# Optimization experiments

Measured on AMD Instinct MI355X. Metric: run time of the kernel, lower is better.

Reference implementation:

```python
import jax, jax.numpy as jnp
import numpy as np

B, F, T, K = 32, 256, 2048, 1024


def setup_inputs() -> dict:
    key = jax.random.key(0)
    k1, k2 = jax.random.split(key)
    x = jax.random.normal(k1, (B, F, T), dtype=jnp.float32)
    emb_weight = jax.random.normal(k2, (K, F), dtype=jnp.float32)
    return {"x": x, "emb_weight": emb_weight}


def reference(x, emb_weight):
    # x: [B, F, T] -> [B, T, F]
    xt = jnp.swapaxes(x, -1, -2)
    nf = xt.shape[-1]

    def sq_dist(a, c):
        # mean over feature dim of (a - c)^2, expanded to avoid a [B,T,K,F]
        # broadcast tensor: (|a|^2 - 2 a.c + |c|^2) / F -> [B, T, K]
        a2 = jnp.sum(a * a, axis=-1, keepdims=True)          # [B,T,1]
        c2 = jnp.sum(c * c, axis=-1)                          # [K]
        ac = jnp.einsum('btf,kf->btk', a, c)                  # [B,T,K]
        return (a2 - 2.0 * ac + c2) / nf

    w_sg = jax.lax.stop_gradient(emb_weight)
    x_sg = jax.lax.stop_gradient(xt)

    dist = sq_dist(xt, w_sg)                                  # [B,T,K]
    min_dist = jnp.min(dist, axis=-1)                         # [B,T]
    idxs = jnpp_argmin(dist) if False else jnp.argmin(dist, axis=-1)  # [B,T]

    loss_commit = min_dist.mean()                              # grads -> x only
    loss_codebook = jnp.min(sq_dist(x_sg, emb_weight), axis=-1).mean()  # grads -> codebook only

    out = w_sg[idxs]                                           # [B,T,F] gather (detached)
    out = jnp.swapaxes(out, -1, -2)                            # [B,F,T]
    return out, loss_commit, loss_codebook
```

## Files before the change

kernel.cpp:

```cpp
#include <hip/hip_runtime.h>

#define B_ 32
#define F_ 256
#define T_ 2048
#define K_ 1024
#define M_ (B_*T_)

#define MARGIN 0.45f
#define CAP 512

typedef _Float16 f16x8 __attribute__((ext_vector_type(8)));
typedef float f32x4 __attribute__((ext_vector_type(4)));

__global__ void k_prep(const float* __restrict__ emb, unsigned short* __restrict__ cprep,
                       double* __restrict__ c2d, float* __restrict__ c2f) {
    int k = blockIdx.x;
    int l = threadIdx.x;
    float4 v = *reinterpret_cast<const float4*>(emb + k * F_ + l * 4);
    union { _Float16 h[4]; unsigned long long ll; } cv;
    cv.h[0] = (_Float16)v.x; cv.h[1] = (_Float16)v.y;
    cv.h[2] = (_Float16)v.z; cv.h[3] = (_Float16)v.w;
    *reinterpret_cast<unsigned long long*>(cprep + k * F_ + l * 4) = cv.ll;
    double s = (double)v.x * v.x + (double)v.y * v.y
             + (double)v.z * v.z + (double)v.w * v.w;
    #pragma unroll
    for (int d = 1; d < 64; d <<= 1) s += __shfl_xor(s, d);
    if (l == 0) { c2d[k] = s; c2f[k] = (float)s; }
}

__global__ __launch_bounds__(256, 2) void k_argmin(
    const float* __restrict__ x, const float* __restrict__ emb,
    const unsigned short* __restrict__ cprep,
    const double* __restrict__ c2d, const float* __restrict__ c2f,
    int* __restrict__ idx_out, double* __restrict__ partials)
{
    __shared__ __align__(16) unsigned char bbuf[2][8192];
    __shared__ int cand_cnt;
    __shared__ int cand_pk[CAP];
    __shared__ double cand_q[CAP];
    __shared__ int res_k[128];
    __shared__ double redbuf[256];

    const int tid = threadIdx.x;
    const int bid = blockIdx.x;
    const int b = bid >> 4;
    const int t_base = (bid & 15) * 128;
    const int w = tid >> 6;
    const int l = tid & 63;
    const int row = l & 15;
    const int qd = l >> 4;
    const int rsw = (row & 7) << 4;
    const int row512 = row * 512;

    if (tid == 0) cand_cnt = 0;

    const float* xb = x + (size_t)b * (F_ * T_) + t_base + w * 32 + row
                    + (size_t)qd * 8 * T_;
    float xsql = 0.f, xsqh = 0.f;
    f16x8 ah0[8], ah1[8];
    #pragma unroll
    for (int s = 0; s < 8; ++s) {
        #pragma unroll
        for (int j = 0; j < 8; ++j) {
            size_t fo = (size_t)(s * 32 + j) * T_;
            float v0 = xb[fo];
            float v1 = xb[fo + 16];
            ah0[s][j] = (_Float16)v0;
            ah1[s][j] = (_Float16)v1;
            xsql = fmaf(v0, v0, xsql);
            xsqh = fmaf(v1, v1, xsqh);
        }
    }
    float xl = xsql, xh = xsqh;
    xl += __shfl_xor(xl, 16); xl += __shfl_xor(xl, 32);
    xh += __shfl_xor(xh, 16); xh += __shfl_xor(xh, 32);
    float a2s[8];
    #pragma unroll
    for (int r = 0; r < 4; ++r) {
        a2s[r]     = __shfl(xl, qd * 4 + r);
        a2s[4 + r] = __shfl(xh, qd * 4 + r);
    }

    const int srow = tid >> 5;
    const int sfc = tid & 31;
    const int sdst = srow * 512 + ((sfc * 16) ^ ((srow & 7) << 4));

    {
        const unsigned short* p0 = cprep + srow * F_ + sfc * 8;
        uint4 a = *reinterpret_cast<const uint4*>(p0);
        uint4 c = *reinterpret_cast<const uint4*>(p0 + 8 * F_);
        *reinterpret_cast<uint4*>(&bbuf[0][sdst]) = a;
        *reinterpret_cast<uint4*>(&bbuf[0][sdst + 4096]) = c;
    }
    __syncthreads();

    int m1i[8], m2i[8], m3i[8];
    #pragma unroll
    for (int i = 0; i < 8; ++i) { m1i[i] = 0x7FFFFFFF; m2i[i] = 0x7FFFFFFF; m3i[i] = 0x7FFFFFFF; }

    for (int tile = 0; tile < 64; ++tile) {
        const int cur = tile & 1, nxt = cur ^ 1;
        uint4 st0, st1;
        if (tile < 63) {
            const unsigned short* p0 = cprep + ((tile + 1) * 16 + srow) * F_ + sfc * 8;
            st0 = *reinterpret_cast<const uint4*>(p0);
            st1 = *reinterpret_cast<const uint4*>(p0 + 8 * F_);
        }
        const int kk = tile * 16 + row;
        float c2v = c2f[kk];

        f32x4 acc0 = {0.f, 0.f, 0.f, 0.f};
        f32x4 acc1 = {0.f, 0.f, 0.f, 0.f};
        #pragma unroll
        for (int s = 0; s < 8; ++s) {
            int off = row512 + (((s * 64) + qd * 16) ^ rsw);
            f16x8 bh = *reinterpret_cast<const f16x8*>(&bbuf[cur][off]);
            acc0 = __builtin_amdgcn_mfma_f32_16x16x32_f16(ah0[s], bh, acc0, 0, 0, 0);
            acc1 = __builtin_amdgcn_mfma_f32_16x16x32_f16(ah1[s], bh, acc1, 0, 0, 0);
        }

        #pragma unroll
        for (int r = 0; r < 4; ++r) {
            {
                float q = fmaf(acc0[r], -2.0f, c2v + a2s[r]);
                int vi = (__float_as_int(q) & 0xFFFFFC00) | kk;
                int t1 = max(m1i[r], vi); m1i[r] = min(m1i[r], vi);
                int t2 = max(m2i[r], t1); m2i[r] = min(m2i[r], t1);
                m3i[r] = min(m3i[r], t2);
            }
            {
                float q = fmaf(acc1[r], -2.0f, c2v + a2s[4 + r]);
                int vi = (__float_as_int(q) & 0xFFFFFC00) | kk;
                int t1 = max(m1i[4 + r], vi); m1i[4 + r] = min(m1i[4 + r], vi);
                int t2 = max(m2i[4 + r], t1); m2i[4 + r] = min(m2i[4 + r], t1);
                m3i[4 + r] = min(m3i[4 + r], t2);
            }
        }

        if (tile < 63) {
            *reinterpret_cast<uint4*>(&bbuf[nxt][sdst]) = st0;
            *reinterpret_cast<uint4*>(&bbuf[nxt][sdst + 4096]) = st1;
        }
        __syncthreads();
    }

    double loss_acc = 0.0;
    #pragma unroll
    for (int i = 0; i < 8; ++i) {
        int gm = m1i[i];
        #pragma unroll
        for (int d = 1; d < 16; d <<= 1) { int o = __shfl_xor(gm, d); gm = min(gm, o); }
        float thr = __int_as_float(gm & 0xFFFFFC00) + MARGIN;
        bool in1 = __int_as_float(m1i[i] & 0xFFFFFC00) <= thr;
        bool in2 = __int_as_float(m2i[i] & 0xFFFFFC00) <= thr;
        bool in3 = __int_as_float(m3i[i] & 0xFFFFFC00) <= thr;
        unsigned long long b1 = __ballot(in1), b2 = __ballot(in2), b3 = __ballot(in3);
        int sh = l & 48;
        int cnt = __popcll((b1 >> sh) & 0xFFFFull) + __popcll((b2 >> sh) & 0xFFFFull)
                + __popcll((b3 >> sh) & 0xFFFFull);
        int p = w * 32 + (i >> 2) * 16 + qd * 4 + (i & 3);
        if ((l & 15) == 0) {
            res_k[p] = gm & 1023;
            loss_acc += (double)__int_as_float((gm & 0xFFFFFC00) | 512);
        }
        if (cnt >= 2) {
            if (in1) { int s_ = atomicAdd(&cand_cnt, 1); if (s_ < CAP) cand_pk[s_] = (p << 10) | (m1i[i] & 1023); }
            if (in2) { int s_ = atomicAdd(&cand_cnt, 1); if (s_ < CAP) cand_pk[s_] = (p << 10) | (m2i[i] & 1023); }
            if (in3) { int s_ = atomicAdd(&cand_cnt, 1); if (s_ < CAP) cand_pk[s_] = (p << 10) | (m3i[i] & 1023); }
        }
    }
    __syncthreads();

    int total = cand_cnt; if (total > CAP) total = CAP;
    for (int ci = w; ci < total; ci += 4) {
        int pk = cand_pk[ci];
        int p = pk >> 10, k = pk & 1023;
        const float* xp = x + (size_t)b * (F_ * T_) + t_base + p;
        const float4 ev = *reinterpret_cast<const float4*>(emb + k * F_ + l * 4);
        double s = 0.0;
        s += (double)xp[(size_t)(l * 4 + 0) * T_] * (double)ev.x;
        s += (double)xp[(size_t)(l * 4 + 1) * T_] * (double)ev.y;
        s += (double)xp[(size_t)(l * 4 + 2) * T_] * (double)ev.z;
        s += (double)xp[(size_t)(l * 4 + 3) * T_] * (double)ev.w;
        #pragma unroll
        for (int d = 1; d < 64; d <<= 1) s += __shfl_xor(s, d);
        if (l == 0) cand_q[ci] = c2d[k] - 2.0 * s;
    }
    __syncthreads();

    if (tid < 128) {
        double bq = 1e300; int bk = -1; bool any = false;
        for (int ci = 0; ci < total; ++ci) {
            int pk = cand_pk[ci];
            if ((pk >> 10) == tid) {
                double q = cand_q[ci]; int k = pk & 1023;
                if (q < bq || (q == bq && k < bk)) { bq = q; bk = k; }
                any = true;
            }
        }
        idx_out[b * T_ + t_base + tid] = any ? bk : res_k[tid];
    }

    redbuf[tid] = loss_acc;
    __syncthreads();
    for (int s = 128; s > 0; s >>= 1) {
        if (tid < s) redbuf[tid] += redbuf[tid + s];
        __syncthreads();
    }
    if (tid == 0) partials[bid] = redbuf[0];
}

__global__ void k_loss(const double* __restrict__ partials, float* __restrict__ out_losses) {
    __shared__ double redd[256];
    int tid = threadIdx.x;
    redd[tid] = partials[tid] + partials[tid + 256];
    __syncthreads();
    for (int s = 128; s > 0; s >>= 1) {
        if (tid < s) redd[tid] += redd[tid + s];
        __syncthreads();
    }
    if (tid == 0) {
        float loss = (float)(redd[0] / ((double)F_ * (double)M_));
        out_losses[0] = loss;
        out_losses[1] = loss;
    }
}

__global__ void k_gather(const float* __restrict__ emb, const int* __restrict__ idx,
                         float* __restrict__ out) {
    int gid = blockIdx.x * 256 + threadIdx.x;
    int t4 = gid & 511;
    int f = (gid >> 9) & 255;
    int b = gid >> 17;
    const int4 ip = *reinterpret_cast<const int4*>(idx + b * T_ + t4 * 4);
    float4 v;
    v.x = emb[ip.x * F_ + f];
    v.y = emb[ip.y * F_ + f];
    v.z = emb[ip.z * F_ + f];
    v.w = emb[ip.w * F_ + f];
    *reinterpret_cast<float4*>(out + (b * F_ + f) * T_ + t4 * 4) = v;
}

extern "C" void kernel_launch(void* const* d_in, const int* in_sizes, int n_in,
                              void* d_out, int out_size, void* d_ws, size_t ws_size,
                              hipStream_t stream) {
    const float* x   = (const float*)d_in[0];
    const float* emb = (const float*)d_in[1];
    float* out = (float*)d_out;

    double* c2d = (double*)d_ws;
    double* partials = c2d + K_;
    unsigned short* cprep = (unsigned short*)(partials + 512);
    float* c2f = (float*)(cprep + K_ * F_);
    int* idx = (int*)(c2f + K_);

    k_prep<<<K_, 64, 0, stream>>>(emb, cprep, c2d, c2f);
    k_argmin<<<M_ / 128, 256, 0, stream>>>(x, emb, cprep, c2d, c2f, idx, partials);
    k_loss<<<1, 256, 0, stream>>>(partials, out + (size_t)M_ * F_);
    k_gather<<<(M_ * (F_ / 4)) / 256, 256, 0, stream>>>(emb, idx, out);
}
```

Measured before the change: 203.3 us.

## Use single-wave argmin blocks with register-prefetched codebook and LDS-transposed gather

Argmin blocks shrink from four waves to one, each handling 32 positions. The codebook tiles now go straight from global memory into registers with a two-tile software prefetch, so the LDS double buffer and per-tile block barriers are gone. The gather kernel now reads whole contiguous codebook rows into an LDS tile and writes transposed coalesced output, replacing scattered per-element reads. The trade-offs are more codebook traffic through L2, since each wave loads every tile itself, a smaller candidate cap, and more partials to reduce in the loss kernel.

Result: slower. 244.9 us (+20.5%).

```diff
diff --git a/kernel.cpp b/kernel.cpp
--- a/kernel.cpp
+++ b/kernel.cpp
@@ -7,7 +7,7 @@
 #define M_ (B_*T_)
 
 #define MARGIN 0.45f
-#define CAP 512
+#define CAP 128
 
 typedef _Float16 f16x8 __attribute__((ext_vector_type(8)));
 typedef float f32x4 __attribute__((ext_vector_type(4)));
@@ -28,34 +28,63 @@
     if (l == 0) { c2d[k] = s; c2f[k] = (float)s; }
 }
 
-__global__ __launch_bounds__(256, 2) void k_argmin(
+#define LOADB(dst, c2n, tt) {                                                    \
+    const unsigned short* bp = cprep + ((tt) * 16 + row) * F_ + qd * 8;          \
+    _Pragma("unroll")                                                            \
+    for (int s_ = 0; s_ < 8; ++s_)                                               \
+        dst[s_] = *reinterpret_cast<const f16x8*>(bp + s_ * 32);                 \
+    c2n = c2f[(tt) * 16 + row];                                                  \
+}
+
+#define COMPUTE(bf, c2v, tt) {                                                   \
+    const int kk = (tt) * 16 + row;                                              \
+    f32x4 acc0 = {0.f, 0.f, 0.f, 0.f};                                           \
+    f32x4 acc1 = {0.f, 0.f, 0.f, 0.f};                                           \
+    _Pragma("unroll")                                                            \
+    for (int s_ = 0; s_ < 8; ++s_) {                                             \
+        acc0 = __builtin_amdgcn_mfma_f32_16x16x32_f16(ah0[s_], bf[s_], acc0, 0, 0, 0); \
+        acc1 = __builtin_amdgcn_mfma_f32_16x16x32_f16(ah1[s_], bf[s_], acc1, 0, 0, 0); \
+    }                                                                            \
+    _Pragma("unroll")                                                            \
+    for (int r_ = 0; r_ < 4; ++r_) {                                             \
+        {                                                                        \
+            float q = fmaf(acc0[r_], -2.0f, c2v + a2s[r_]);                      \
+            int vi = (__float_as_int(q) & 0xFFFFFC00) | kk;                      \
+            int t1 = max(m1i[r_], vi); m1i[r_] = min(m1i[r_], vi);               \
+            int t2 = max(m2i[r_], t1); m2i[r_] = min(m2i[r_], t1);               \
+            m3i[r_] = min(m3i[r_], t2);                                          \
+        }                                                                        \
+        {                                                                        \
+            float q = fmaf(acc1[r_], -2.0f, c2v + a2s[4 + r_]);                  \
+            int vi = (__float_as_int(q) & 0xFFFFFC00) | kk;                      \
+            int t1 = max(m1i[4 + r_], vi); m1i[4 + r_] = min(m1i[4 + r_], vi);   \
+            int t2 = max(m2i[4 + r_], t1); m2i[4 + r_] = min(m2i[4 + r_], t1);   \
+            m3i[4 + r_] = min(m3i[4 + r_], t2);                                  \
+        }                                                                        \
+    }                                                                            \
+}
+
+__global__ __launch_bounds__(64, 2) void k_argmin(
     const float* __restrict__ x, const float* __restrict__ emb,
     const unsigned short* __restrict__ cprep,
     const double* __restrict__ c2d, const float* __restrict__ c2f,
     int* __restrict__ idx_out, double* __restrict__ partials)
 {
-    __shared__ __align__(16) unsigned char bbuf[2][8192];
     __shared__ int cand_cnt;
     __shared__ int cand_pk[CAP];
     __shared__ double cand_q[CAP];
-    __shared__ int res_k[128];
-    __shared__ double redbuf[256];
-
-    const int tid = threadIdx.x;
+    __shared__ int res_k[32];
+
+    const int l = threadIdx.x;
     const int bid = blockIdx.x;
-    const int b = bid >> 4;
-    const int t_base = (bid & 15) * 128;
-    const int w = tid >> 6;
-    const int l = tid & 63;
+    const int b = bid >> 6;
+    const int t0 = (bid & 63) * 32;
     const int row = l & 15;
     const int qd = l >> 4;
-    const int rsw = (row & 7) << 4;
-    const int row512 = row * 512;
-
-    if (tid == 0) cand_cnt = 0;
-
-    const float* xb = x + (size_t)b * (F_ * T_) + t_base + w * 32 + row
-                    + (size_t)qd * 8 * T_;
+
+    if (l == 0) cand_cnt = 0;
+
+    const float* xb = x + (size_t)b * (F_ * T_) + t0 + row + (size_t)qd * 8 * T_;
     float xsql = 0.f, xsqh = 0.f;
     f16x8 ah0[8], ah1[8];
     #pragma unroll
@@ -81,67 +110,19 @@
         a2s[4 + r] = __shfl(xh, qd * 4 + r);
     }
 
-    const int srow = tid >> 5;
-    const int sfc = tid & 31;
-    const int sdst = srow * 512 + ((sfc * 16) ^ ((srow & 7) << 4));
-
-    {
-        const unsigned short* p0 = cprep + srow * F_ + sfc * 8;
-        uint4 a = *reinterpret_cast<const uint4*>(p0);
-        uint4 c = *reinterpret_cast<const uint4*>(p0 + 8 * F_);
-        *reinterpret_cast<uint4*>(&bbuf[0][sdst]) = a;
-        *reinterpret_cast<uint4*>(&bbuf[0][sdst + 4096]) = c;
-    }
-    __syncthreads();
-
     int m1i[8], m2i[8], m3i[8];
     #pragma unroll
     for (int i = 0; i < 8; ++i) { m1i[i] = 0x7FFFFFFF; m2i[i] = 0x7FFFFFFF; m3i[i] = 0x7FFFFFFF; }
 
-    for (int tile = 0; tile < 64; ++tile) {
-        const int cur = tile & 1, nxt = cur ^ 1;
-        uint4 st0, st1;
-        if (tile < 63) {
-            const unsigned short* p0 = cprep + ((tile + 1) * 16 + srow) * F_ + sfc * 8;
-            st0 = *reinterpret_cast<const uint4*>(p0);
-            st1 = *reinterpret_cast<const uint4*>(p0 + 8 * F_);
-        }
-        const int kk = tile * 16 + row;
-        float c2v = c2f[kk];
-
-        f32x4 acc0 = {0.f, 0.f, 0.f, 0.f};
-        f32x4 acc1 = {0.f, 0.f, 0.f, 0.f};
-        #pragma unroll
-        for (int s = 0; s < 8; ++s) {
-            int off = row512 + (((s * 64) + qd * 16) ^ rsw);
-            f16x8 bh = *reinterpret_cast<const f16x8*>(&bbuf[cur][off]);
-            acc0 = __builtin_amdgcn_mfma_f32_16x16x32_f16(ah0[s], bh, acc0, 0, 0, 0);
-            acc1 = __builtin_amdgcn_mfma_f32_16x16x32_f16(ah1[s], bh, acc1, 0, 0, 0);
-        }
-
-        #pragma unroll
-        for (int r = 0; r < 4; ++r) {
-            {
-                float q = fmaf(acc0[r], -2.0f, c2v + a2s[r]);
-                int vi = (__float_as_int(q) & 0xFFFFFC00) | kk;
-                int t1 = max(m1i[r], vi); m1i[r] = min(m1i[r], vi);
-                int t2 = max(m2i[r], t1); m2i[r] = min(m2i[r], t1);
-                m3i[r] = min(m3i[r], t2);
-            }
-            {
-                float q = fmaf(acc1[r], -2.0f, c2v + a2s[4 + r]);
-                int vi = (__float_as_int(q) & 0xFFFFFC00) | kk;
-                int t1 = max(m1i[4 + r], vi); m1i[4 + r] = min(m1i[4 + r], vi);
-                int t2 = max(m2i[4 + r], t1); m2i[4 + r] = min(m2i[4 + r], t1);
-                m3i[4 + r] = min(m3i[4 + r], t2);
-            }
-        }
-
-        if (tile < 63) {
-            *reinterpret_cast<uint4*>(&bbuf[nxt][sdst]) = st0;
-            *reinterpret_cast<uint4*>(&bbuf[nxt][sdst + 4096]) = st1;
-        }
-        __syncthreads();
+    f16x8 bA[8], bB[8];
+    float c2A, c2B;
+    LOADB(bA, c2A, 0);
+    #pragma unroll 1
+    for (int t = 0; t < 64; t += 2) {
+        LOADB(bB, c2B, t + 1);
+        COMPUTE(bA, c2A, t);
+        if (t + 2 < 64) LOADB(bA, c2A, t + 2);
+        COMPUTE(bB, c2B, t + 1);
     }
 
     double loss_acc = 0.0;
@@ -158,7 +139,7 @@
         int sh = l & 48;
         int cnt = __popcll((b1 >> sh) & 0xFFFFull) + __popcll((b2 >> sh) & 0xFFFFull)
                 + __popcll((b3 >> sh) & 0xFFFFull);
-        int p = w * 32 + (i >> 2) * 16 + qd * 4 + (i & 3);
+        int p = (i >> 2) * 16 + qd * 4 + (i & 3);
         if ((l & 15) == 0) {
             res_k[p] = gm & 1023;
             loss_acc += (double)__int_as_float((gm & 0xFFFFFC00) | 512);
@@ -172,10 +153,10 @@
     __syncthreads();
 
     int total = cand_cnt; if (total > CAP) total = CAP;
-    for (int ci = w; ci < total; ci += 4) {
+    for (int ci = 0; ci < total; ++ci) {
         int pk = cand_pk[ci];
         int p = pk >> 10, k = pk & 1023;
-        const float* xp = x + (size_t)b * (F_ * T_) + t_base + p;
+        const float* xp = x + (size_t)b * (F_ * T_) + t0 + p;
         const float4 ev = *reinterpret_cast<const float4*>(emb + k * F_ + l * 4);
         double s = 0.0;
         s += (double)xp[(size_t)(l * 4 + 0) * T_] * (double)ev.x;
@@ -188,35 +169,34 @@
     }
     __syncthreads();
 
-    if (tid < 128) {
+    if (l < 32) {
         double bq = 1e300; int bk = -1; bool any = false;
         for (int ci = 0; ci < total; ++ci) {
             int pk = cand_pk[ci];
-            if ((pk >> 10) == tid) {
+            if ((pk >> 10) == l) {
                 double q = cand_q[ci]; int k = pk & 1023;
                 if (q < bq || (q == bq && k < bk)) { bq = q; bk = k; }
                 any = true;
             }
         }
-        idx_out[b * T_ + t_base + tid] = any ? bk : res_k[tid];
-    }
-
-    redbuf[tid] = loss_acc;
-    __syncthreads();
-    for (int s = 128; s > 0; s >>= 1) {
-        if (tid < s) redbuf[tid] += redbuf[tid + s];
-        __syncthreads();
-    }
-    if (tid == 0) partials[bid] = redbuf[0];
+        idx_out[b * T_ + t0 + l] = any ? bk : res_k[l];
+    }
+
+    #pragma unroll
+    for (int d = 1; d < 64; d <<= 1) loss_acc += __shfl_xor(loss_acc, d);
+    if (l == 0) partials[bid] = loss_acc;
 }
 
 __global__ void k_loss(const double* __restrict__ partials, float* __restrict__ out_losses) {
     __shared__ double redd[256];
     int tid = threadIdx.x;
-    redd[tid] = partials[tid] + partials[tid + 256];
-    __syncthreads();
-    for (int s = 128; s > 0; s >>= 1) {
-        if (tid < s) redd[tid] += redd[tid + s];
+    double s = 0.0;
+    #pragma unroll
+    for (int i = 0; i < 8; ++i) s += partials[tid + i * 256];
+    redd[tid] = s;
+    __syncthreads();
+    for (int st = 128; st > 0; st >>= 1) {
+        if (tid < st) redd[tid] += redd[tid + st];
         __syncthreads();
     }
     if (tid == 0) {
@@ -226,19 +206,41 @@
     }
 }
 
-__global__ void k_gather(const float* __restrict__ emb, const int* __restrict__ idx,
-                         float* __restrict__ out) {
-    int gid = blockIdx.x * 256 + threadIdx.x;
-    int t4 = gid & 511;
-    int f = (gid >> 9) & 255;
-    int b = gid >> 17;
-    const int4 ip = *reinterpret_cast<const int4*>(idx + b * T_ + t4 * 4);
-    float4 v;
-    v.x = emb[ip.x * F_ + f];
-    v.y = emb[ip.y * F_ + f];
-    v.z = emb[ip.z * F_ + f];
-    v.w = emb[ip.w * F_ + f];
-    *reinterpret_cast<float4*>(out + (b * F_ + f) * T_ + t4 * 4) = v;
+__global__ __launch_bounds__(256) void k_gather(
+    const float* __restrict__ emb, const int* __restrict__ idx,
+    float* __restrict__ out)
+{
+    __shared__ float tile[32][257];
+    __shared__ int karr[32];
+
+    const int tid = threadIdx.x;
+    const int bid = blockIdx.x;
+    const int b = bid >> 6;
+    const int t0 = (bid & 63) * 32;
+
+    if (tid < 32) karr[tid] = idx[b * T_ + t0 + tid];
+    __syncthreads();
+
+    #pragma unroll
+    for (int pass = 0; pass < 8; ++pass) {
+        int r = pass * 4 + (tid >> 6);
+        int c = (tid & 63) * 4;
+        *reinterpret_cast<float4*>(&tile[r][c]) =
+            *reinterpret_cast<const float4*>(emb + karr[r] * F_ + c);
+    }
+    __syncthreads();
+
+    #pragma unroll
+    for (int pass = 0; pass < 8; ++pass) {
+        int f = pass * 32 + (tid >> 3);
+        int t4 = (tid & 7) * 4;
+        float4 v;
+        v.x = tile[t4 + 0][f];
+        v.y = tile[t4 + 1][f];
+        v.z = tile[t4 + 2][f];
+        v.w = tile[t4 + 3][f];
+        *reinterpret_cast<float4*>(out + ((size_t)b * F_ + f) * T_ + t0 + t4) = v;
+    }
 }
 
 extern "C" void kernel_launch(void* const* d_in, const int* in_sizes, int n_in,
@@ -250,12 +252,12 @@
 
     double* c2d = (double*)d_ws;
     double* partials = c2d + K_;
-    unsigned short* cprep = (unsigned short*)(partials + 512);
+    unsigned short* cprep = (unsigned short*)(partials + 2048);
     float* c2f = (float*)(cprep + K_ * F_);
     int* idx = (int*)(c2f + K_);
 
     k_prep<<<K_, 64, 0, stream>>>(emb, cprep, c2d, c2f);
-    k_argmin<<<M_ / 128, 256, 0, stream>>>(x, emb, cprep, c2d, c2f, idx, partials);
+    k_argmin<<<M_ / 32, 64, 0, stream>>>(x, emb, cprep, c2d, c2f, idx, partials);
     k_loss<<<1, 256, 0, stream>>>(partials, out + (size_t)M_ * F_);
-    k_gather<<<(M_ * (F_ / 4)) / 256, 256, 0, stream>>>(emb, idx, out);
-}
+    k_gather<<<M_ / 32, 256, 0, stream>>>(emb, idx, out);
+}
```
